# Optimization experiments

Hardware: AMD Instinct MI355X
Metric: run time of the kernel (lower is better)

## Reference

```python
import jax, jax.numpy as jnp
import numpy as np
from jax import lax

B, T, K = 64, 2048, 128


def setup_inputs() -> dict:
    key = jax.random.key(0)
    k0, k1, k2, k3, k4, k5 = jax.random.split(key, 6)
    emissions = jax.random.normal(k0, (B, T, K), dtype=jnp.float32)
    lengths = jax.random.randint(k1, (B,), T // 2, T + 1)
    mask = jnp.arange(T)[None, :] < lengths[:, None]  # left-aligned [B,T] bool
    target = jax.random.bernoulli(k2, 0.5, (B, T, K))  # supervision set [B,T,K] bool
    forbidden_transitions = jax.random.bernoulli(k3, 0.1, (K, K))
    transitions = jax.random.normal(k4, (K, K), dtype=jnp.float32) * 0.01
    start_transitions = jax.random.normal(k5, (K,), dtype=jnp.float32) * 0.01
    return dict(emissions=emissions, mask=mask, target=target,
                transitions=transitions, start_transitions=start_transitions,
                forbidden_transitions=forbidden_transitions)


def reference(emissions, mask, target, transitions, start_transitions, forbidden_transitions):
    # Faithful to torch forward: transitions masked with -10000; end_transitions unused;
    # raw (unmasked) start_transitions added to EVERY timestep (as in the source).
    trans = jnp.where(forbidden_transitions, jnp.float32(-10000.0), transitions)  # [K,K]
    sup_em = jnp.where(target, emissions, jnp.float32(-100000.0))  # masked_fill(~target)
    bi = jnp.concatenate([sup_em, emissions], axis=0)  # [2B,T,K]
    bi = bi + start_transitions  # broadcast over all timesteps (source quirk)

    alpha0 = bi[:, 0]  # [2B,K]

    def step(alpha, em_t):
        # logdotexp: logsumexp_i(alpha[:,i] + trans[i,j]) + em_t[:,j]
        new = jax.nn.logsumexp(alpha[:, :, None] + trans[None, :, :], axis=1) + em_t
        return new, new

    _, outs = lax.scan(step, alpha0, jnp.swapaxes(bi[:, 1:], 0, 1))  # [T-1,2B,K]
    outs = jnp.concatenate([alpha0[None], outs], axis=0)  # [T,2B,K]

    lengths = mask.sum(-1)  # [B]
    last = jnp.concatenate([lengths, lengths]) - 1  # [2B]
    z_alpha = outs[last, jnp.arange(2 * B)]  # alpha at last valid step, [2B,K]
    z = jax.nn.logsumexp(z_alpha, axis=-1)  # [2B]
    supervised_z = z[:B]
    unsupervised_z = z[B:]
    return supervised_z - unsupervised_z
```

## Files before the change

### kernel.cpp

```cpp
#include <hip/hip_runtime.h>
#include <stdint.h>

#define BB 64
#define TT 2048
#define KK 128
#define QSTRIDE 40

typedef float f32x16 __attribute__((ext_vector_type(16)));
typedef float f32x2  __attribute__((ext_vector_type(2)));

__device__ __forceinline__ float waveMax(float v) {
#pragma unroll
    for (int off = 32; off; off >>= 1) v = fmaxf(v, __shfl_xor(v, off, 64));
    return v;
}
__device__ __forceinline__ float waveSum(float v) {
#pragma unroll
    for (int off = 32; off; off >>= 1) v += __shfl_xor(v, off, 64);
    return v;
}
__device__ __forceinline__ int waveSumI(int v) {
#pragma unroll
    for (int off = 32; off; off >>= 1) v += __shfl_xor(v, off, 64);
    return v;
}
__device__ __forceinline__ float quadSum(float s) {
    int x = __builtin_amdgcn_mov_dpp(__float_as_int(s), 0xB1, 0xf, 0xf, true);
    s += __int_as_float(x);
    x = __builtin_amdgcn_mov_dpp(__float_as_int(s), 0x4E, 0xf, 0xf, true);
    s += __int_as_float(x);
    return s;
}
__device__ __forceinline__ float waveMaxFast(float v) {
    int x = __builtin_amdgcn_mov_dpp(__float_as_int(v), 0xB1, 0xf, 0xf, true);
    v = fmaxf(v, __int_as_float(x));
    x = __builtin_amdgcn_mov_dpp(__float_as_int(v), 0x4E, 0xf, 0xf, true);
    v = fmaxf(v, __int_as_float(x));
#pragma unroll
    for (int off = 4; off <= 32; off <<= 1) v = fmaxf(v, __shfl_xor(v, off, 64));
    return v;
}

__device__ __forceinline__ void lds_barrier() {
    asm volatile("s_waitcnt lgkmcnt(0)\n\ts_barrier" ::: "memory");
}

#define PKFMA(ep, wp, acc) acc = __builtin_elementwise_fma(ep, wp, acc)

#define MATVEC_QUARTER(Wa, Wb, ev, sOut) {                          \
    const float4 e0 = ev[0], e1 = ev[1], e2 = ev[2], e3 = ev[3];    \
    const float4 e4 = ev[4], e5 = ev[5], e6 = ev[6], e7 = ev[7];    \
    f32x2 a0 = {0.f,0.f}, a1 = {0.f,0.f}, a2 = {0.f,0.f}, a3 = {0.f,0.f}; \
    PKFMA(((f32x2){e0.x, e0.y}), ((f32x2){Wa[0],  Wa[1]}),  a0);    \
    PKFMA(((f32x2){e0.z, e0.w}), ((f32x2){Wa[2],  Wa[3]}),  a1);    \
    PKFMA(((f32x2){e1.x, e1.y}), ((f32x2){Wa[4],  Wa[5]}),  a2);    \
    PKFMA(((f32x2){e1.z, e1.w}), ((f32x2){Wa[6],  Wa[7]}),  a3);    \
    PKFMA(((f32x2){e2.x, e2.y}), ((f32x2){Wa[8],  Wa[9]}),  a0);    \
    PKFMA(((f32x2){e2.z, e2.w}), ((f32x2){Wa[10], Wa[11]}), a1);    \
    PKFMA(((f32x2){e3.x, e3.y}), ((f32x2){Wa[12], Wa[13]}), a2);    \
    PKFMA(((f32x2){e3.z, e3.w}), ((f32x2){Wa[14], Wa[15]}), a3);    \
    PKFMA(((f32x2){e4.x, e4.y}), ((f32x2){Wb[0],  Wb[1]}),  a0);    \
    PKFMA(((f32x2){e4.z, e4.w}), ((f32x2){Wb[2],  Wb[3]}),  a1);    \
    PKFMA(((f32x2){e5.x, e5.y}), ((f32x2){Wb[4],  Wb[5]}),  a2);    \
    PKFMA(((f32x2){e5.z, e5.w}), ((f32x2){Wb[6],  Wb[7]}),  a3);    \
    PKFMA(((f32x2){e6.x, e6.y}), ((f32x2){Wb[8],  Wb[9]}),  a0);    \
    PKFMA(((f32x2){e6.z, e6.w}), ((f32x2){Wb[10], Wb[11]}), a1);    \
    PKFMA(((f32x2){e7.x, e7.y}), ((f32x2){Wb[12], Wb[13]}), a2);    \
    PKFMA(((f32x2){e7.z, e7.w}), ((f32x2){Wb[14], Wb[15]}), a3);    \
    const f32x2 s2 = (a0 + a1) + (a2 + a3);                         \
    sOut = s2[0] + s2[1]; }

extern "C" __global__ __launch_bounds__(512)
void crf_fb_kernel(const float* __restrict__ em,
                   const int* __restrict__ mask,
                   const int* __restrict__ tgt,
                   const float* __restrict__ trans,
                   const float* __restrict__ start,
                   const int* __restrict__ forb,
                   float* __restrict__ ef,
                   float* __restrict__ db,
                   float* __restrict__ Mfb)
{
    const int tid  = threadIdx.x;
    const int k    = tid >> 2;
    const int q    = tid & 3;
    const int w    = tid >> 6;
    const int lane = tid & 63;
    const bool fwdDir = (blockIdx.x < 2 * BB);
    const int c    = blockIdx.x & (2 * BB - 1);
    const int b    = c & (BB - 1);
    const bool sup = (c < BB);

    __shared__ __align__(16) float eLDS[2][3 * QSTRIDE + 32];
    __shared__ float wmLDS[8];
    __shared__ float redLDS[8];
    __shared__ int lenLDS;

    if (tid == 0) lenLDS = 0;
    const int4 m4 = ((const int4*)(mask + (size_t)b * TT))[tid];
    int ps = m4.x + m4.y + m4.z + m4.w;
    ps = waveSumI(ps);
    __syncthreads();
    if (lane == 0) atomicAdd(&lenLDS, ps);

    const float st = start[k];
    const float* __restrict__ emrow = em + (size_t)b * TT * KK;
    const int* __restrict__ trow = tgt + (size_t)b * TT * KK;

    const int ib = q * 32;
    f32x16 Wa, Wb;
    if (fwdDir) {
#pragma unroll
        for (int j = 0; j < 16; ++j) {
            Wa[j] = forb[(ib + j     ) * KK + k] ? 0.0f : __expf(trans[(ib + j     ) * KK + k]);
            Wb[j] = forb[(ib + 16 + j) * KK + k] ? 0.0f : __expf(trans[(ib + 16 + j) * KK + k]);
        }
    } else {
#pragma unroll
        for (int j = 0; j < 16; ++j) {
            Wa[j] = forb[k * KK + ib + j     ] ? 0.0f : __expf(trans[k * KK + ib + j     ]);
            Wb[j] = forb[k * KK + ib + 16 + j] ? 0.0f : __expf(trans[k * KK + ib + 16 + j]);
        }
    }
    __syncthreads();
    const int len = lenLDS;
    const int mid = len >> 1;
    const int N   = fwdDir ? mid : (len - 1 - mid);
    const int t0  = fwdDir ? 0 : (len - 1);

    float v0 = emrow[(size_t)t0 * KK + k];
    if (sup && !trow[(size_t)t0 * KK + k]) v0 = -100000.0f;
    v0 += st;
    const float wm0 = waveMax(v0);
    if (lane == 0) redLDS[w] = wm0;
    __syncthreads();
    float M0 = fmaxf(fmaxf(fmaxf(redLDS[0], redLDS[1]), fmaxf(redLDS[2], redLDS[3])),
                     fmaxf(fmaxf(redLDS[4], redLDS[5]), fmaxf(redLDS[6], redLDS[7])));
    double M = (double)M0;
    float eNew = __expf(v0 - M0);
    if (q == 0) eLDS[0][(k >> 5) * QSTRIDE + (k & 31)] = eNew;

    auto bival = [&](int t) -> float {
        float e0 = emrow[(size_t)t * KK + k];
        if (sup) { if (!trow[(size_t)t * KK + k]) e0 = -100000.0f; }
        return e0 + st;
    };
    auto loadBi = [&](int n) -> float {
        if (n > N || (!fwdDir && n == N)) return 0.0f;
        const int t = fwdDir ? n : (len - 1 - n);
        return bival(t);
    };

    float biA = loadBi(1), biB = loadBi(2), biC = loadBi(3), biD = loadBi(4);
    float sPrev = 1.0f, baPrev = 0.0f;
    lds_barrier();

#pragma unroll 4
    for (int n = 1; n <= N; ++n) {
        const int p = (n - 1) & 1;
        const float biN = loadBi(n + 4);

        if ((n & 3) == 3) {
            const float u = __logf(sPrev) + baPrev;
            const float wmx = waveMaxFast(u);
            if (lane == 0) wmLDS[w] = wmx;
        }
        float r = 0.0f;
        if ((n & 3) == 0) {
            r = fmaxf(fmaxf(fmaxf(wmLDS[0], wmLDS[1]), fmaxf(wmLDS[2], wmLDS[3])),
                      fmaxf(fmaxf(wmLDS[4], wmLDS[5]), fmaxf(wmLDS[6], wmLDS[7])));
            M += (double)r;
        }
        const float ba = biA - r;
        const float f = __expf(ba);

        const float4* __restrict__ ev = (const float4*)(&eLDS[p][q * QSTRIDE]);
        float s;
        MATVEC_QUARTER(Wa, Wb, ev, s)
        s = quadSum(s);

        eNew = s * f;
        if (q == 0) eLDS[p ^ 1][(k >> 5) * QSTRIDE + (k & 31)] = eNew;

        sPrev = s; baPrev = ba;
        biA = biB; biB = biC; biC = biD; biD = biN;
        lds_barrier();
    }

    if (q == 0) { (fwdDir ? ef : db)[(size_t)c * KK + k] = eNew; }
    if (tid == 0) Mfb[(fwdDir ? 0 : 2 * BB) + c] = (float)M;
}

extern "C" __global__ void crf_combine_kernel(const float* __restrict__ ef,
                                              const float* __restrict__ db,
                                              const float* __restrict__ Mfb,
                                              float* __restrict__ out)
{
    const int b = blockIdx.x;
    const int tid = threadIdx.x;
    const int wv = tid >> 6, lane = tid & 63;
    __shared__ float red[2][2];
    __shared__ float z[2];
#pragma unroll
    for (int s = 0; s < 2; ++s) {
        const int c = b + s * BB;
        const float v = ef[(size_t)c * KK + tid] * db[(size_t)c * KK + tid];
        const float p = waveSum(v);
        if (lane == 0) red[s][wv] = p;
    }
    __syncthreads();
    if (tid < 2) {
        const int c = b + tid * BB;
        z[tid] = Mfb[c] + Mfb[2 * BB + c] + __logf(red[tid][0] + red[tid][1]);
    }
    __syncthreads();
    if (tid == 0) out[b] = z[0] - z[1];
}

extern "C" __global__ __launch_bounds__(512)
__attribute__((amdgpu_waves_per_eu(2, 2)))
void crf_chain_kernel(const float* __restrict__ em, const int* __restrict__ mask,
                      const int* __restrict__ tgt, const float* __restrict__ trans,
                      const float* __restrict__ start, const int* __restrict__ forb,
                      float* __restrict__ zbuf)
{
    const int tid = threadIdx.x;
    const int k = tid >> 2, q = tid & 3, w = tid >> 6, lane = tid & 63;
    const int c = blockIdx.x, b = c & (BB - 1);
    const bool sup = (c < BB);
    __shared__ __align__(16) float eLDS[2][KK];
    __shared__ float wmLDS[8];
    __shared__ float redLDS[8];
    __shared__ int lenLDS;
    if (tid == 0) lenLDS = 0;
    const int4 m4 = ((const int4*)(mask + (size_t)b * TT))[tid];
    int ps = m4.x + m4.y + m4.z + m4.w;
    ps = waveSumI(ps);
    __syncthreads();
    if (lane == 0) atomicAdd(&lenLDS, ps);
    const float st = start[k];
    const float* __restrict__ emrow = em + (size_t)b * TT * KK;
    const int* __restrict__ trow = tgt + (size_t)b * TT * KK;
    const int ib = q * 32;
    f32x16 Wa, Wb;
#pragma unroll
    for (int j = 0; j < 16; ++j) {
        Wa[j] = forb[(ib + j     ) * KK + k] ? 0.0f : __expf(trans[(ib + j     ) * KK + k]);
        Wb[j] = forb[(ib + 16 + j) * KK + k] ? 0.0f : __expf(trans[(ib + 16 + j) * KK + k]);
    }
    float v0 = emrow[k];
    if (sup && !trow[k]) v0 = -100000.0f;
    v0 += st;
    const float wm0 = waveMax(v0);
    if (lane == 0) redLDS[w] = wm0;
    __syncthreads();
    const int len = lenLDS;
    float M0 = fmaxf(fmaxf(fmaxf(redLDS[0], redLDS[1]), fmaxf(redLDS[2], redLDS[3])),
                     fmaxf(fmaxf(redLDS[4], redLDS[5]), fmaxf(redLDS[6], redLDS[7])));
    double M = (double)M0;
    float eNew = __expf(v0 - M0);
    if (q == 0) eLDS[0][k] = eNew;
    auto bival = [&](int t) -> float {
        float e0 = emrow[(size_t)t * KK + k];
        if (sup) { if (!trow[(size_t)t * KK + k]) e0 = -100000.0f; }
        return e0 + st;
    };
    float biA = (len > 1) ? bival(1) : 0.0f;
    float biB = (len > 2) ? bival(2) : 0.0f;
    float biC = (len > 3) ? bival(3) : 0.0f;
    float biD = (len > 4) ? bival(4) : 0.0f;
    float sPrev = 1.0f, baPrev = 0.0f;
    lds_barrier();
#pragma unroll 4
    for (int t = 1; t < len; ++t) {
        const int p = (t - 1) & 1;
        const float biN = (t + 4 < len) ? bival(t + 4) : 0.0f;
        if ((t & 3) == 3) {
            const float u = __logf(sPrev) + baPrev;
            const float wmx = waveMaxFast(u);
            if (lane == 0) wmLDS[w] = wmx;
        }
        float r = 0.0f;
        if ((t & 3) == 0) {
            r = fmaxf(fmaxf(fmaxf(wmLDS[0], wmLDS[1]), fmaxf(wmLDS[2], wmLDS[3])),
                      fmaxf(fmaxf(wmLDS[4], wmLDS[5]), fmaxf(wmLDS[6], wmLDS[7])));
            M += (double)r;
        }
        const float ba = biA - r;
        const float f = __expf(ba);
        const float4* __restrict__ ev = (const float4*)eLDS[p] + q * 8;
        float s;
        MATVEC_QUARTER(Wa, Wb, ev, s)
        s = quadSum(s);
        eNew = s * f;
        if (q == 0) eLDS[p ^ 1][k] = eNew;
        sPrev = s; baPrev = ba;
        biA = biB; biB = biC; biC = biD; biD = biN;
        lds_barrier();
    }
    const float sm = waveSum((q == 0) ? eNew : 0.0f);
    if (lane == 0) redLDS[w] = sm;
    __syncthreads();
    if (tid == 0) {
        const float ss = ((redLDS[0] + redLDS[1]) + (redLDS[2] + redLDS[3]))
                       + ((redLDS[4] + redLDS[5]) + (redLDS[6] + redLDS[7]));
        zbuf[c] = (float)(M + (double)__logf(ss));
    }
}

extern "C" __global__ void crf_final_kernel(const float* __restrict__ z,
                                            float* __restrict__ out)
{
    const int b = threadIdx.x;
    out[b] = z[b] - z[b + BB];
}

extern "C" void kernel_launch(void* const* d_in, const int* in_sizes, int n_in,
                              void* d_out, int out_size, void* d_ws, size_t ws_size,
                              hipStream_t stream) {
    const float* em    = (const float*)d_in[0];
    const int*   mask  = (const int*)d_in[1];
    const int*   tgt   = (const int*)d_in[2];
    const float* trans = (const float*)d_in[3];
    const float* start = (const float*)d_in[4];
    const int*   forb  = (const int*)d_in[5];

    const size_t need = (size_t)(2 * 2 * BB * KK + 4 * BB) * sizeof(float);
    if (ws_size >= need) {
        float* ef  = (float*)d_ws;
        float* db  = ef + 2 * BB * KK;
        float* Mfb = db + 2 * BB * KK;
        crf_fb_kernel<<<4 * BB, 512, 0, stream>>>(em, mask, tgt, trans, start,
                                                  forb, ef, db, Mfb);
        crf_combine_kernel<<<BB, 128, 0, stream>>>(ef, db, Mfb, (float*)d_out);
    } else {
        float* zbuf = (float*)d_ws;
        crf_chain_kernel<<<2 * BB, 512, 0, stream>>>(em, mask, tgt, trans, start,
                                                     forb, zbuf);
        crf_final_kernel<<<1, BB, 0, stream>>>(zbuf, (float*)d_out);
    }
}
```

Before: 933.6 us.

## Re-tile CRF matvec so each 16-lane group computes four output states

Reorganises the per-step matrix-vector product. Each thread used to own one output state with a 32-element slice of the input. Now each 16-lane group owns four output states, and each thread handles an 8-element input slice for all four, with a reduction across 16 lanes done through DPP row operations. Emissions and targets are loaded as float4/int4 vectors, and the periodic max rescale uses the max of the current values through DPP-only reductions instead of a log of the sum. The goal is fewer LDS reads per FMA and shorter cross-lane reduction latency on the serial recurrence, at the cost of more DPP adds per step and a changed LDS padding layout.

After: 1.124 ms. 1.2x slower.

```diff
diff --git a/kernel.cpp b/kernel.cpp
--- a/kernel.cpp
+++ b/kernel.cpp
@@ -38,6 +38,31 @@
     v = fmaxf(v, __int_as_float(x));
 #pragma unroll
     for (int off = 4; off <= 32; off <<= 1) v = fmaxf(v, __shfl_xor(v, off, 64));
+    return v;
+}
+
+template<int C> __device__ __forceinline__ float dppMax(float v) {
+    int x = __builtin_amdgcn_mov_dpp(__float_as_int(v), C, 0xf, 0xf, true);
+    return fmaxf(v, __int_as_float(x));
+}
+template<int C> __device__ __forceinline__ float dppAdd(float v) {
+    int x = __builtin_amdgcn_mov_dpp(__float_as_int(v), C, 0xf, 0xf, true);
+    return v + __int_as_float(x);
+}
+__device__ __forceinline__ float red16(float s) {
+    s = dppAdd<0xB1>(s);
+    s = dppAdd<0x4E>(s);
+    s = dppAdd<0x124>(s);
+    s = dppAdd<0x128>(s);
+    return s;
+}
+__device__ __forceinline__ float waveMaxTo63(float v) {
+    v = dppMax<0xB1>(v);
+    v = dppMax<0x4E>(v);
+    v = dppMax<0x124>(v);
+    v = dppMax<0x128>(v);
+    v = dppMax<0x142>(v);
+    v = dppMax<0x143>(v);
     return v;
 }
 
@@ -82,8 +107,10 @@
                    float* __restrict__ Mfb)
 {
     const int tid  = threadIdx.x;
-    const int k    = tid >> 2;
-    const int q    = tid & 3;
+    const int G    = tid >> 4;
+    const int ig   = tid & 15;
+    const int k0   = G << 2;
+    const int i0   = ig << 3;
     const int w    = tid >> 6;
     const int lane = tid & 63;
     const bool fwdDir = (blockIdx.x < 2 * BB);
@@ -91,7 +118,7 @@
     const int b    = c & (BB - 1);
     const bool sup = (c < BB);
 
-    __shared__ __align__(16) float eLDS[2][3 * QSTRIDE + 32];
+    __shared__ __align__(16) float eLDS[2][144];
     __shared__ float wmLDS[8];
     __shared__ float redLDS[8];
     __shared__ int lenLDS;
@@ -103,24 +130,27 @@
     __syncthreads();
     if (lane == 0) atomicAdd(&lenLDS, ps);
 
-    const float st = start[k];
+    const float4 st4 = *(const float4*)(start + k0);
     const float* __restrict__ emrow = em + (size_t)b * TT * KK;
     const int* __restrict__ trow = tgt + (size_t)b * TT * KK;
 
-    const int ib = q * 32;
-    f32x16 Wa, Wb;
+    float Wv[4][8];
     if (fwdDir) {
 #pragma unroll
-        for (int j = 0; j < 16; ++j) {
-            Wa[j] = forb[(ib + j     ) * KK + k] ? 0.0f : __expf(trans[(ib + j     ) * KK + k]);
-            Wb[j] = forb[(ib + 16 + j) * KK + k] ? 0.0f : __expf(trans[(ib + 16 + j) * KK + k]);
-        }
+        for (int r = 0; r < 4; ++r)
+#pragma unroll
+            for (int j = 0; j < 8; ++j) {
+                const int idx = (i0 + j) * KK + (k0 + r);
+                Wv[r][j] = forb[idx] ? 0.0f : __expf(trans[idx]);
+            }
     } else {
 #pragma unroll
-        for (int j = 0; j < 16; ++j) {
-            Wa[j] = forb[k * KK + ib + j     ] ? 0.0f : __expf(trans[k * KK + ib + j     ]);
-            Wb[j] = forb[k * KK + ib + 16 + j] ? 0.0f : __expf(trans[k * KK + ib + 16 + j]);
-        }
+        for (int r = 0; r < 4; ++r)
+#pragma unroll
+            for (int j = 0; j < 8; ++j) {
+                const int idx = (k0 + r) * KK + (i0 + j);
+                Wv[r][j] = forb[idx] ? 0.0f : __expf(trans[idx]);
+            }
     }
     __syncthreads();
     const int len = lenLDS;
@@ -128,66 +158,100 @@
     const int N   = fwdDir ? mid : (len - 1 - mid);
     const int t0  = fwdDir ? 0 : (len - 1);
 
-    float v0 = emrow[(size_t)t0 * KK + k];
-    if (sup && !trow[(size_t)t0 * KK + k]) v0 = -100000.0f;
-    v0 += st;
-    const float wm0 = waveMax(v0);
+    const int rb = i0 + ((ig >> 2) << 2);
+    const int cw = G >> 1;
+    const int wb = (cw << 3) + ((cw >> 2) << 2) + ((G & 1) << 2);
+
+    float4 v0 = *(const float4*)(emrow + (size_t)t0 * KK + k0);
+    if (sup) {
+        const int4 t4 = *(const int4*)(trow + (size_t)t0 * KK + k0);
+        v0.x = t4.x ? v0.x : -100000.0f;
+        v0.y = t4.y ? v0.y : -100000.0f;
+        v0.z = t4.z ? v0.z : -100000.0f;
+        v0.w = t4.w ? v0.w : -100000.0f;
+    }
+    v0.x += st4.x; v0.y += st4.y; v0.z += st4.z; v0.w += st4.w;
+    const float vmax = fmaxf(fmaxf(v0.x, v0.y), fmaxf(v0.z, v0.w));
+    const float wm0 = waveMax(vmax);
     if (lane == 0) redLDS[w] = wm0;
     __syncthreads();
     float M0 = fmaxf(fmaxf(fmaxf(redLDS[0], redLDS[1]), fmaxf(redLDS[2], redLDS[3])),
                      fmaxf(fmaxf(redLDS[4], redLDS[5]), fmaxf(redLDS[6], redLDS[7])));
     double M = (double)M0;
-    float eNew = __expf(v0 - M0);
-    if (q == 0) eLDS[0][(k >> 5) * QSTRIDE + (k & 31)] = eNew;
-
-    auto bival = [&](int t) -> float {
-        float e0 = emrow[(size_t)t * KK + k];
-        if (sup) { if (!trow[(size_t)t * KK + k]) e0 = -100000.0f; }
-        return e0 + st;
+    float4 eNewV;
+    eNewV.x = __expf(v0.x - M0);
+    eNewV.y = __expf(v0.y - M0);
+    eNewV.z = __expf(v0.z - M0);
+    eNewV.w = __expf(v0.w - M0);
+    if (ig == 0) *(float4*)&eLDS[0][wb] = eNewV;
+
+    auto loadBi = [&](int n) -> float4 {
+        if (n > N || (!fwdDir && n == N)) return make_float4(0.f, 0.f, 0.f, 0.f);
+        const int t = fwdDir ? n : (len - 1 - n);
+        float4 e4 = *(const float4*)(emrow + (size_t)t * KK + k0);
+        if (sup) {
+            const int4 t4 = *(const int4*)(trow + (size_t)t * KK + k0);
+            e4.x = t4.x ? e4.x : -100000.0f;
+            e4.y = t4.y ? e4.y : -100000.0f;
+            e4.z = t4.z ? e4.z : -100000.0f;
+            e4.w = t4.w ? e4.w : -100000.0f;
+        }
+        e4.x += st4.x; e4.y += st4.y; e4.z += st4.z; e4.w += st4.w;
+        return e4;
     };
-    auto loadBi = [&](int n) -> float {
-        if (n > N || (!fwdDir && n == N)) return 0.0f;
-        const int t = fwdDir ? n : (len - 1 - n);
-        return bival(t);
-    };
-
-    float biA = loadBi(1), biB = loadBi(2), biC = loadBi(3), biD = loadBi(4);
-    float sPrev = 1.0f, baPrev = 0.0f;
+
+    float4 biA = loadBi(1), biB = loadBi(2), biC = loadBi(3), biD = loadBi(4);
     lds_barrier();
+
+#define FMA8(ar, Wr) {                                              \
+    PKFMA(((f32x2){e0.x, e0.y}), ((f32x2){Wr[0], Wr[1]}), ar);      \
+    PKFMA(((f32x2){e0.z, e0.w}), ((f32x2){Wr[2], Wr[3]}), ar);      \
+    PKFMA(((f32x2){e1.x, e1.y}), ((f32x2){Wr[4], Wr[5]}), ar);      \
+    PKFMA(((f32x2){e1.z, e1.w}), ((f32x2){Wr[6], Wr[7]}), ar); }
 
 #pragma unroll 4
     for (int n = 1; n <= N; ++n) {
         const int p = (n - 1) & 1;
-        const float biN = loadBi(n + 4);
+        const float4 biN = loadBi(n + 4);
 
         if ((n & 3) == 3) {
-            const float u = __logf(sPrev) + baPrev;
-            const float wmx = waveMaxFast(u);
-            if (lane == 0) wmLDS[w] = wmx;
+            const float mprev = fmaxf(fmaxf(eNewV.x, eNewV.y), fmaxf(eNewV.z, eNewV.w));
+            const float u = waveMaxTo63(__logf(mprev));
+            if (lane == 63) wmLDS[w] = u;
         }
         float r = 0.0f;
         if ((n & 3) == 0) {
-            r = fmaxf(fmaxf(fmaxf(wmLDS[0], wmLDS[1]), fmaxf(wmLDS[2], wmLDS[3])),
-                      fmaxf(fmaxf(wmLDS[4], wmLDS[5]), fmaxf(wmLDS[6], wmLDS[7])));
+            float rv = wmLDS[lane & 7];
+            rv = dppMax<0xB1>(rv);
+            rv = dppMax<0x4E>(rv);
+            rv = dppMax<0x124>(rv);
+            r = rv;
             M += (double)r;
         }
-        const float ba = biA - r;
-        const float f = __expf(ba);
-
-        const float4* __restrict__ ev = (const float4*)(&eLDS[p][q * QSTRIDE]);
-        float s;
-        MATVEC_QUARTER(Wa, Wb, ev, s)
-        s = quadSum(s);
-
-        eNew = s * f;
-        if (q == 0) eLDS[p ^ 1][(k >> 5) * QSTRIDE + (k & 31)] = eNew;
-
-        sPrev = s; baPrev = ba;
+        const float f0 = __expf(biA.x - r);
+        const float f1 = __expf(biA.y - r);
+        const float f2 = __expf(biA.z - r);
+        const float f3 = __expf(biA.w - r);
+
+        const float4* __restrict__ ev = (const float4*)&eLDS[p][rb];
+        const float4 e0 = ev[0], e1 = ev[1];
+
+        f32x2 a0 = {0.f,0.f}, a1 = {0.f,0.f}, a2 = {0.f,0.f}, a3 = {0.f,0.f};
+        FMA8(a0, Wv[0]); FMA8(a1, Wv[1]); FMA8(a2, Wv[2]); FMA8(a3, Wv[3]);
+        float s0 = a0[0] + a0[1];
+        float s1 = a1[0] + a1[1];
+        float s2 = a2[0] + a2[1];
+        float s3 = a3[0] + a3[1];
+        s0 = red16(s0); s1 = red16(s1); s2 = red16(s2); s3 = red16(s3);
+
+        eNewV.x = s0 * f0; eNewV.y = s1 * f1; eNewV.z = s2 * f2; eNewV.w = s3 * f3;
+        if (ig == 0) *(float4*)&eLDS[p ^ 1][wb] = eNewV;
+
         biA = biB; biB = biC; biC = biD; biD = biN;
         lds_barrier();
     }
 
-    if (q == 0) { (fwdDir ? ef : db)[(size_t)c * KK + k] = eNew; }
+    if (ig == 0) *(float4*)((fwdDir ? ef : db) + (size_t)c * KK + k0) = eNewV;
     if (tid == 0) Mfb[(fwdDir ? 0 : 2 * BB) + c] = (float)M;
 }
 
```

## Use one thread per state with full 128-wide row in registers

Applied to the files above, without the earlier changes.

Restructures the forward/backward CRF kernel from 4 threads per state (512-thread blocks) to one thread per state (128-thread blocks). Each thread now holds all 128 transition weights in registers, which removes the quad DPP reduction and shrinks the per-step block barrier to 2 waves. The running max is now taken with a DPP-only reduction to lane 63. The trade-off is four times more serial FMA work per thread on each step, plus heavy register pressure, against cheaper synchronisation across fewer waves.

New measurement: 1.115 ms. +19.5%, slower.

```diff
diff --git a/kernel.cpp b/kernel.cpp
--- a/kernel.cpp
+++ b/kernel.cpp
@@ -4,7 +4,6 @@
 #define BB 64
 #define TT 2048
 #define KK 128
-#define QSTRIDE 40
 
 typedef float f32x16 __attribute__((ext_vector_type(16)));
 typedef float f32x2  __attribute__((ext_vector_type(2)));
@@ -38,6 +37,20 @@
     v = fmaxf(v, __int_as_float(x));
 #pragma unroll
     for (int off = 4; off <= 32; off <<= 1) v = fmaxf(v, __shfl_xor(v, off, 64));
+    return v;
+}
+
+template<int C> __device__ __forceinline__ float dppMax(float v) {
+    int x = __builtin_amdgcn_mov_dpp(__float_as_int(v), C, 0xf, 0xf, true);
+    return fmaxf(v, __int_as_float(x));
+}
+__device__ __forceinline__ float waveMaxTo63(float v) {
+    v = dppMax<0xB1>(v);
+    v = dppMax<0x4E>(v);
+    v = dppMax<0x124>(v);
+    v = dppMax<0x128>(v);
+    v = dppMax<0x142>(v);
+    v = dppMax<0x143>(v);
     return v;
 }
 
@@ -70,7 +83,7 @@
     const f32x2 s2 = (a0 + a1) + (a2 + a3);                         \
     sOut = s2[0] + s2[1]; }
 
-extern "C" __global__ __launch_bounds__(512)
+extern "C" __global__ __launch_bounds__(128, 1)
 void crf_fb_kernel(const float* __restrict__ em,
                    const int* __restrict__ mask,
                    const int* __restrict__ tgt,
@@ -82,8 +95,7 @@
                    float* __restrict__ Mfb)
 {
     const int tid  = threadIdx.x;
-    const int k    = tid >> 2;
-    const int q    = tid & 3;
+    const int k    = tid;
     const int w    = tid >> 6;
     const int lane = tid & 63;
     const bool fwdDir = (blockIdx.x < 2 * BB);
@@ -91,14 +103,19 @@
     const int b    = c & (BB - 1);
     const bool sup = (c < BB);
 
-    __shared__ __align__(16) float eLDS[2][3 * QSTRIDE + 32];
-    __shared__ float wmLDS[8];
-    __shared__ float redLDS[8];
+    __shared__ __align__(16) float eLDS[2][KK];
+    __shared__ __align__(8)  float wmLDS[2];
+    __shared__ float redLDS[2];
     __shared__ int lenLDS;
 
     if (tid == 0) lenLDS = 0;
-    const int4 m4 = ((const int4*)(mask + (size_t)b * TT))[tid];
-    int ps = m4.x + m4.y + m4.z + m4.w;
+    int ps = 0;
+    const int4* __restrict__ mrow = (const int4*)(mask + (size_t)b * TT);
+#pragma unroll
+    for (int it = 0; it < 4; ++it) {
+        const int4 m4 = mrow[tid + 128 * it];
+        ps += m4.x + m4.y + m4.z + m4.w;
+    }
     ps = waveSumI(ps);
     __syncthreads();
     if (lane == 0) atomicAdd(&lenLDS, ps);
@@ -107,19 +124,21 @@
     const float* __restrict__ emrow = em + (size_t)b * TT * KK;
     const int* __restrict__ trow = tgt + (size_t)b * TT * KK;
 
-    const int ib = q * 32;
-    f32x16 Wa, Wb;
+    f32x2 W2[64];
     if (fwdDir) {
 #pragma unroll
-        for (int j = 0; j < 16; ++j) {
-            Wa[j] = forb[(ib + j     ) * KK + k] ? 0.0f : __expf(trans[(ib + j     ) * KK + k]);
-            Wb[j] = forb[(ib + 16 + j) * KK + k] ? 0.0f : __expf(trans[(ib + 16 + j) * KK + k]);
+        for (int j = 0; j < 64; ++j) {
+            const int i0 = 2 * j, i1 = 2 * j + 1;
+            const float w0 = forb[i0 * KK + k] ? 0.0f : __expf(trans[i0 * KK + k]);
+            const float w1 = forb[i1 * KK + k] ? 0.0f : __expf(trans[i1 * KK + k]);
+            W2[j] = (f32x2){w0, w1};
         }
     } else {
 #pragma unroll
-        for (int j = 0; j < 16; ++j) {
-            Wa[j] = forb[k * KK + ib + j     ] ? 0.0f : __expf(trans[k * KK + ib + j     ]);
-            Wb[j] = forb[k * KK + ib + 16 + j] ? 0.0f : __expf(trans[k * KK + ib + 16 + j]);
+        for (int j = 0; j < 64; ++j) {
+            const float w0 = forb[k * KK + 2 * j    ] ? 0.0f : __expf(trans[k * KK + 2 * j    ]);
+            const float w1 = forb[k * KK + 2 * j + 1] ? 0.0f : __expf(trans[k * KK + 2 * j + 1]);
+            W2[j] = (f32x2){w0, w1};
         }
     }
     __syncthreads();
@@ -134,25 +153,20 @@
     const float wm0 = waveMax(v0);
     if (lane == 0) redLDS[w] = wm0;
     __syncthreads();
-    float M0 = fmaxf(fmaxf(fmaxf(redLDS[0], redLDS[1]), fmaxf(redLDS[2], redLDS[3])),
-                     fmaxf(fmaxf(redLDS[4], redLDS[5]), fmaxf(redLDS[6], redLDS[7])));
+    const float M0 = fmaxf(redLDS[0], redLDS[1]);
     double M = (double)M0;
     float eNew = __expf(v0 - M0);
-    if (q == 0) eLDS[0][(k >> 5) * QSTRIDE + (k & 31)] = eNew;
-
-    auto bival = [&](int t) -> float {
+    eLDS[0][k] = eNew;
+
+    auto loadBi = [&](int n) -> float {
+        if (n > N || (!fwdDir && n == N)) return 0.0f;
+        const int t = fwdDir ? n : (len - 1 - n);
         float e0 = emrow[(size_t)t * KK + k];
         if (sup) { if (!trow[(size_t)t * KK + k]) e0 = -100000.0f; }
         return e0 + st;
     };
-    auto loadBi = [&](int n) -> float {
-        if (n > N || (!fwdDir && n == N)) return 0.0f;
-        const int t = fwdDir ? n : (len - 1 - n);
-        return bival(t);
-    };
 
     float biA = loadBi(1), biB = loadBi(2), biC = loadBi(3), biD = loadBi(4);
-    float sPrev = 1.0f, baPrev = 0.0f;
     lds_barrier();
 
 #pragma unroll 4
@@ -161,33 +175,42 @@
         const float biN = loadBi(n + 4);
 
         if ((n & 3) == 3) {
-            const float u = __logf(sPrev) + baPrev;
-            const float wmx = waveMaxFast(u);
-            if (lane == 0) wmLDS[w] = wmx;
+            const float u = waveMaxTo63(__logf(eNew));
+            if (lane == 63) wmLDS[w] = u;
         }
         float r = 0.0f;
         if ((n & 3) == 0) {
-            r = fmaxf(fmaxf(fmaxf(wmLDS[0], wmLDS[1]), fmaxf(wmLDS[2], wmLDS[3])),
-                      fmaxf(fmaxf(wmLDS[4], wmLDS[5]), fmaxf(wmLDS[6], wmLDS[7])));
+            const float2 wmv = *(const float2*)wmLDS;
+            r = fmaxf(wmv.x, wmv.y);
             M += (double)r;
         }
-        const float ba = biA - r;
-        const float f = __expf(ba);
-
-        const float4* __restrict__ ev = (const float4*)(&eLDS[p][q * QSTRIDE]);
-        float s;
-        MATVEC_QUARTER(Wa, Wb, ev, s)
-        s = quadSum(s);
+        const float f = __expf(biA - r);
+
+        const float4* __restrict__ ev = (const float4*)eLDS[p];
+        f32x2 a0 = {0.f,0.f}, a1 = {0.f,0.f}, a2 = {0.f,0.f}, a3 = {0.f,0.f};
+#pragma unroll
+        for (int j = 0; j < 32; j += 4) {
+            const float4 E0 = ev[j], E1 = ev[j + 1], E2 = ev[j + 2], E3 = ev[j + 3];
+            PKFMA(((f32x2){E0.x, E0.y}), W2[2 * j    ], a0);
+            PKFMA(((f32x2){E0.z, E0.w}), W2[2 * j + 1], a1);
+            PKFMA(((f32x2){E1.x, E1.y}), W2[2 * j + 2], a2);
+            PKFMA(((f32x2){E1.z, E1.w}), W2[2 * j + 3], a3);
+            PKFMA(((f32x2){E2.x, E2.y}), W2[2 * j + 4], a0);
+            PKFMA(((f32x2){E2.z, E2.w}), W2[2 * j + 5], a1);
+            PKFMA(((f32x2){E3.x, E3.y}), W2[2 * j + 6], a2);
+            PKFMA(((f32x2){E3.z, E3.w}), W2[2 * j + 7], a3);
+        }
+        const f32x2 aa = (a0 + a1) + (a2 + a3);
+        const float s = aa[0] + aa[1];
 
         eNew = s * f;
-        if (q == 0) eLDS[p ^ 1][(k >> 5) * QSTRIDE + (k & 31)] = eNew;
-
-        sPrev = s; baPrev = ba;
+        eLDS[p ^ 1][k] = eNew;
+
         biA = biB; biB = biC; biC = biD; biD = biN;
         lds_barrier();
     }
 
-    if (q == 0) { (fwdDir ? ef : db)[(size_t)c * KK + k] = eNew; }
+    (fwdDir ? ef : db)[(size_t)c * KK + k] = eNew;
     if (tid == 0) Mfb[(fwdDir ? 0 : 2 * BB) + c] = (float)M;
 }
 
@@ -330,7 +353,7 @@
         float* ef  = (float*)d_ws;
         float* db  = ef + 2 * BB * KK;
         float* Mfb = db + 2 * BB * KK;
-        crf_fb_kernel<<<4 * BB, 512, 0, stream>>>(em, mask, tgt, trans, start,
+        crf_fb_kernel<<<4 * BB, 128, 0, stream>>>(em, mask, tgt, trans, start,
                                                   forb, ef, db, Mfb);
         crf_combine_kernel<<<BB, 128, 0, stream>>>(ef, db, Mfb, (float*)d_out);
     } else {
```
